# Kernel tuning notes

Hardware: AMD Instinct MI355X
Metric: run time of the kernel (lower is better)

## Reference

```python
import jax, jax.numpy as jnp
import numpy as np

NEG_INF = -jnp.inf


def setup_inputs() -> dict:
    B, T, E, H = 16, 1024, 1024, 1024  # batch, seq, embed_dim, head_dim (T <= H required by original buffer slicing)
    key = jax.random.key(0)
    k1, k2, k3, k4, k5, k6 = jax.random.split(key, 6)
    return {
        "key": jax.random.normal(k1, (B, T, E), dtype=jnp.float32),
        "query": jax.random.normal(k2, (B, T, E), dtype=jnp.float32),
        "value": jax.random.normal(k3, (B, T, E), dtype=jnp.float32),
        "padding_mask": jnp.zeros((B, 1, T), dtype=jnp.int32),
        # nn.Linear(embed_dim, head_dim, bias=False) weights: [head_dim, embed_dim]
        "Wk": jax.random.normal(k4, (H, E), dtype=jnp.float32) * (E ** -0.5),
        "Wq": jax.random.normal(k5, (H, E), dtype=jnp.float32) * (E ** -0.5),
        "Wv": jax.random.normal(k6, (H, E), dtype=jnp.float32) * (E ** -0.5),
    }


def reference(key, query, value, padding_mask, Wk, Wq, Wv):
    # key/query/value: [B, T, E]; W*: [H, E]
    B, T, E = key.shape
    k = jnp.einsum("bte,he->bth", key, Wk)
    q = jnp.einsum("bte,he->bth", query, Wq)
    v = jnp.einsum("bte,he->bth", value, Wv)
    # NOTE: original scales by d_k = key.size(-1) = embed_dim, not head_dim
    scale = 1.0 / jnp.sqrt(jnp.float32(E))
    qk = jnp.einsum("bth,bsh->bts", q, k) * scale  # [B, T, T]
    # causal buffer is tril(ones, diagonal=1): position i can attend to j <= i+1
    causal = jnp.tril(jnp.ones((T, T), dtype=jnp.float32), k=1)
    qk = jnp.where(causal == 0, NEG_INF, qk)
    qk = jnp.where(padding_mask == 1, NEG_INF, qk)  # padding_mask broadcasts [B,1,T] -> [B,T,T]
    p = jax.nn.softmax(qk, axis=-1)
    attn = jnp.einsum("bts,bsh->bth", p, v)  # dropout is identity in eval mode
    return attn
```

## Files before the change

### kernel.cpp

```cpp
#include <hip/hip_runtime.h>
#include <hip/hip_bf16.h>
#include <stdint.h>

typedef __bf16 bf16;
typedef __attribute__((ext_vector_type(8))) __bf16 bf16x8;
typedef __attribute__((ext_vector_type(4))) __bf16 bf16x4;
typedef __attribute__((ext_vector_type(4))) float  f32x4;

static __device__ __forceinline__ void gll16(const void* g, void* lds_base) {
  __builtin_amdgcn_global_load_lds((__attribute__((address_space(1))) void*)g,
                                   (__attribute__((address_space(3))) void*)lds_base,
                                   16, 0, 0);
}

#define BARR  __builtin_amdgcn_s_barrier()
#define VMW(N) asm volatile("s_waitcnt vmcnt(" #N ")" ::: "memory")
#define LGKM0 do { asm volatile("s_waitcnt lgkmcnt(0)" ::: "memory");          \
                   __builtin_amdgcn_sched_barrier(0); } while (0)

__global__ __launch_bounds__(512, 2) void proj8(const bf16* __restrict__ a0,
                                                const bf16* __restrict__ a1,
                                                const bf16* __restrict__ b0,
                                                const bf16* __restrict__ b1,
                                                bf16* __restrict__ c0,
                                                bf16* __restrict__ c1) {
  extern __shared__ char smem[];
  char* ldsA = smem;
  char* ldsB = smem + 65536;

  const int tid = threadIdx.x;
  const int lane = tid & 63, wave = tid >> 6;
  const int lo = lane & 15, hi = lane >> 4;
  const int wmi = wave >> 2, wni = wave & 3;
  const int swz = (lo & 7) << 4;

  const int nwg = gridDim.x;
  const int id = (blockIdx.x % 8) * (nwg >> 3) + blockIdx.x / 8;
  const int seg = id >> 8, idl = id & 255;
  const int row0 = (idl >> 2) * 256, col0 = (idl & 3) * 256;
  const bf16* Ap = (seg ? a1 : a0) + (size_t)row0 * 1024;
  const bf16* Bp = (seg ? b1 : b0) + (size_t)col0 * 1024;
  bf16* Cb = seg ? c1 : c0;

  const char* aSrc[2];
  const char* bSrc[2];
  int ldsOff[2];
#pragma unroll
  for (int rr = 0; rr < 2; ++rr) {
    const int x = rr * 8192 + tid * 16;
    const int lr = x >> 7;
    const int colx = (x & 127) ^ ((lr & 7) << 4);
    aSrc[rr] = (const char*)Ap + (size_t)(((lr >> 6) << 7) | (lr & 63)) * 2048 + colx;
    bSrc[rr] = (const char*)Bp + (size_t)(((lr >> 5) << 6) | (lr & 31)) * 2048 + colx;
    ldsOff[rr] = rr * 8192 + wave * 1024;
  }
  auto stA = [&](int h, int buf, int t) {
    const int tc = t > 15 ? 15 : t;
#pragma unroll
    for (int rr = 0; rr < 2; ++rr)
      gll16(aSrc[rr] + h * 131072 + tc * 128,
            ldsA + buf * 32768 + h * 16384 + ldsOff[rr]);
  };
  auto stB = [&](int h, int buf, int t) {
    const int tc = t > 15 ? 15 : t;
#pragma unroll
    for (int rr = 0; rr < 2; ++rr)
      gll16(bSrc[rr] + h * 65536 + tc * 128,
            ldsB + buf * 32768 + h * 16384 + ldsOff[rr]);
  };

  f32x4 acc[8][4] = {};
  bf16x8 af[4][2], bq0[2][2], bq1[2][2];

  auto rdA = [&](int mq, int buf) {
#pragma unroll
    for (int i = 0; i < 4; ++i) {
      const int lr = wmi * 64 + i * 16 + lo;
#pragma unroll
      for (int kh = 0; kh < 2; ++kh)
        af[i][kh] = *(const bf16x8*)(ldsA + buf * 32768 + mq * 16384 +
                                     lr * 128 + ((kh * 64 + hi * 16) ^ swz));
    }
  };
  auto rdB = [&](bf16x8 bq[2][2], int nq, int buf) {
#pragma unroll
    for (int n = 0; n < 2; ++n) {
      const int lr = wni * 32 + n * 16 + lo;
#pragma unroll
      for (int kh = 0; kh < 2; ++kh)
        bq[n][kh] = *(const bf16x8*)(ldsB + buf * 32768 + nq * 16384 +
                                     lr * 128 + ((kh * 64 + hi * 16) ^ swz));
    }
  };
  auto mma = [&](bf16x8 bq[2][2], int mq, int nq) {
    __builtin_amdgcn_s_setprio(1);
#pragma unroll
    for (int i = 0; i < 4; ++i)
#pragma unroll
      for (int n = 0; n < 2; ++n)
#pragma unroll
        for (int kh = 0; kh < 2; ++kh)
          acc[mq * 4 + i][nq * 2 + n] = __builtin_amdgcn_mfma_f32_16x16x32_bf16(
              af[i][kh], bq[n][kh], acc[mq * 4 + i][nq * 2 + n], 0, 0, 0);
    __builtin_amdgcn_s_setprio(0);
  };

  stA(0, 0, 0); stB(1, 0, 0); stA(1, 0, 0); stB(0, 0, 0);
  stA(0, 1, 1); stB(1, 1, 1); stA(1, 1, 1);
  VMW(6); BARR;

  for (int j = 0; j < 8; ++j) {
    const int t1 = 2 * j + 1, t2 = 2 * j + 2, t3 = 2 * j + 3;
    rdA(0, 0); rdB(bq0, 0, 0); stB(0, 1, t1);
    BARR; LGKM0; mma(bq0, 0, 0); BARR;
    rdB(bq1, 1, 0); stA(0, 0, t2);
    BARR; LGKM0; mma(bq1, 0, 1); BARR;
    rdA(1, 0); stB(1, 0, t2);
    BARR; LGKM0; mma(bq1, 1, 1); BARR;
    stA(1, 0, t2);
    BARR; LGKM0; mma(bq0, 1, 0); VMW(6); BARR;
    rdA(0, 1); rdB(bq0, 0, 1); stB(0, 0, t2);
    BARR; LGKM0; mma(bq0, 0, 0); BARR;
    rdB(bq1, 1, 1); stA(0, 1, t3);
    BARR; LGKM0; mma(bq1, 0, 1); BARR;
    rdA(1, 1); stB(1, 1, t3);
    BARR; LGKM0; mma(bq1, 1, 1); BARR;
    stA(1, 1, t3);
    BARR; LGKM0; mma(bq0, 1, 0); VMW(6); BARR;
  }

  if (!seg) {
#pragma unroll
    for (int m = 0; m < 8; ++m)
#pragma unroll
      for (int n = 0; n < 4; ++n) {
        const int c = col0 + wni * 64 + n * 16 + lo;
        const int rbase = row0 + wmi * 128 + m * 16 + hi * 4;
#pragma unroll
        for (int j = 0; j < 4; ++j)
          Cb[(size_t)(rbase + j) * 1024 + c] = (bf16)acc[m][n][j];
      }
  } else {
#pragma unroll
    for (int m = 0; m < 8; ++m)
#pragma unroll
      for (int n = 0; n < 4; ++n) {
        const int r = row0 + wmi * 128 + m * 16 + hi * 4;
        const int c = col0 + wni * 64 + n * 16 + lo;
        const int bb = r >> 10, tt = r & 1023;
        bf16x4 h = { (bf16)acc[m][n][0], (bf16)acc[m][n][1],
                     (bf16)acc[m][n][2], (bf16)acc[m][n][3] };
        *(bf16x4*)(Cb + ((size_t)bb << 20) + ((size_t)c << 10) + tt) = h;
      }
  }
  asm volatile("s_waitcnt vmcnt(0)" ::: "memory");
}

template <int VARIANT>
__global__ __launch_bounds__(512, 2) void gemm8(const bf16* __restrict__ a0,
                                                const bf16* __restrict__ b0,
                                                bf16* __restrict__ c0,
                                                float* __restrict__ Cf,
                                                const int* __restrict__ pad) {
  constexpr int TM = (VARIANT == 0) ? 256 : 128;
  constexpr int TN = (VARIANT == 0) ? 256 : 128;
  constexpr int ABYTES = TM * 64;
  constexpr int BBYTES = TN * 64;
  constexpr int AROUNDS = ABYTES / 8192;
  constexpr int BROUNDS = BBYTES / 8192;
  constexpr int FI = TM / 64;
  constexpr int FN = TN / 64;
  extern __shared__ char smem[];
  char* ldsA = smem;
  char* ldsB = smem + 2 * ABYTES;

  const int tid = threadIdx.x;
  const int lane = tid & 63, wave = tid >> 6;
  const int lo = lane & 15, hi = lane >> 4;
  const int wmi = wave >> 2, wni = wave & 3;
  const int swz = ((lo >> 1) & 3) << 4;

  const int nwg = gridDim.x;
  const int id = (blockIdx.x % 8) * (nwg >> 3) + blockIdx.x / 8;

  int row0, col0, nt, batch = 0;
  const bf16 *Ap, *Bp;
  bf16* Cb;
  if (VARIANT == 0) {
    const int idl = id & 255;
    row0 = (idl >> 2) * 256; col0 = (idl & 3) * 256; nt = 32;
    Ap = a0 + (size_t)row0 * 1024;
    Bp = b0 + (size_t)col0 * 1024;
    Cb = c0;
  } else {
    batch = id >> 6;
    const int it = (id >> 3) & 7, jt = id & 7;
    row0 = it * 128; col0 = jt * 128;
    nt = (VARIANT == 3) ? min(32, 4 * it + 5) : 32;
    if (VARIANT == 2 && jt >= it + 2) {
      bf16* Sb = c0 + ((size_t)batch << 20);
      bf16x8 z = {};
#pragma unroll
      for (int q = 0; q < (TM * TN) / (512 * 8); ++q) {
        const int off = (q * 512 + tid) * 8;
        *(bf16x8*)(Sb + (size_t)(row0 + (off >> 7)) * 1024 + col0 + (off & 127)) = z;
      }
      return;
    }
    Ap = a0 + ((size_t)batch << 20) + (size_t)row0 * 1024;
    Bp = b0 + ((size_t)batch << 20) + (size_t)col0 * 1024;
    Cb = c0;
  }
  const int ntm1 = nt - 1;

  auto stgA = [&](int tidx, int slot) {
    const int tc = tidx > ntm1 ? ntm1 : tidx;
#pragma unroll
    for (int r = 0; r < AROUNDS; ++r) {
      const int x  = (r * 512 + tid) * 16;
      const int xs = x ^ (((x >> 7) & 3) << 4);
      gll16((const char*)Ap + (size_t)(xs >> 6) * 2048 + (size_t)tc * 64 + (xs & 63),
            ldsA + slot * ABYTES + r * 8192 + wave * 1024);
    }
  };
  auto stgB = [&](int tidx, int slot) {
    const int tc = tidx > ntm1 ? ntm1 : tidx;
#pragma unroll
    for (int r = 0; r < BROUNDS; ++r) {
      const int x  = (r * 512 + tid) * 16;
      const int xs = x ^ (((x >> 7) & 3) << 4);
      gll16((const char*)Bp + (size_t)(xs >> 6) * 2048 + (size_t)tc * 64 + (xs & 63),
            ldsB + slot * BBYTES + r * 8192 + wave * 1024);
    }
  };

  f32x4 acc[2 * FI][FN] = {};
  bf16x8 af[FI], bfr[FN];

  auto rdA = [&](int mh, int slot) {
#pragma unroll
    for (int i = 0; i < FI; ++i) {
      const int row = wmi * (TM / 2) + mh * (TM / 4) + i * 16 + lo;
      af[i] = *(const bf16x8*)(ldsA + slot * ABYTES + ((row * 64 + hi * 16) ^ swz));
    }
  };
  auto rdB = [&](int slot) {
#pragma unroll
    for (int n = 0; n < FN; ++n) {
      const int row = wni * (TN / 4) + n * 16 + lo;
      bfr[n] = *(const bf16x8*)(ldsB + slot * BBYTES + ((row * 64 + hi * 16) ^ swz));
    }
  };
  auto mmaQ = [&](int mh) {
    __builtin_amdgcn_s_setprio(1);
#pragma unroll
    for (int i = 0; i < FI; ++i)
#pragma unroll
      for (int n = 0; n < FN; ++n)
        acc[mh * FI + i][n] = __builtin_amdgcn_mfma_f32_16x16x32_bf16(
            af[i], bfr[n], acc[mh * FI + i][n], 0, 0, 0);
    __builtin_amdgcn_s_setprio(0);
  };

  stgB(0, 0);
  stgA(0, 0);
  stgB(1, 1);
  if constexpr (BROUNDS == 2) { VMW(2); } else { VMW(1); }
  BARR;

#pragma unroll 2
  for (int u = 0; u < nt; ++u) {
    const int cur = u & 1;
    rdA(0, cur);
    rdB(cur);
    stgA(u + 1, cur ^ 1);
    BARR; LGKM0;
    mmaQ(0);
    BARR;
    rdA(1, cur);
    stgB(u + 2, cur);
    BARR; LGKM0;
    mmaQ(1);
    if constexpr (BROUNDS == 2) { VMW(2); } else { VMW(1); }
    BARR;
  }

  if (VARIANT == 0) {
#pragma unroll
    for (int m = 0; m < 2 * FI; ++m)
#pragma unroll
      for (int n = 0; n < FN; ++n) {
        const int c = col0 + wni * (TN / 4) + n * 16 + lo;
        const int rbase = row0 + wmi * (TM / 2) + m * 16 + hi * 4;
#pragma unroll
        for (int j = 0; j < 4; ++j)
          Cb[(size_t)(rbase + j) * 1024 + c] = (bf16)acc[m][n][j];
      }
  } else if (VARIANT == 2) {
    const float NINF = -__builtin_inff();
#pragma unroll
    for (int n = 0; n < FN; ++n) {
      const int s = col0 + wni * (TN / 4) + n * 16 + lo;
      const int pd = pad[(batch << 10) + s];
#pragma unroll
      for (int m = 0; m < 2 * FI; ++m) {
        const int tbase = row0 + wmi * (TM / 2) + m * 16 + hi * 4;
#pragma unroll
        for (int j = 0; j < 4; ++j) {
          float v = acc[m][n][j] * 0.03125f;
          if (s > tbase + j + 1) v = 0.f;
          else if (pd != 0) v = NINF;
          Cb[((size_t)batch << 20) + (size_t)(tbase + j) * 1024 + s] = (bf16)v;
        }
      }
    }
  } else {
#pragma unroll
    for (int m = 0; m < 2 * FI; ++m)
#pragma unroll
      for (int n = 0; n < FN; ++n) {
        const int h2 = col0 + wni * (TN / 4) + n * 16 + lo;
        const int tbase = row0 + wmi * (TM / 2) + m * 16 + hi * 4;
#pragma unroll
        for (int j = 0; j < 4; ++j)
          Cf[((size_t)batch << 20) + (size_t)(tbase + j) * 1024 + h2] = acc[m][n][j];
      }
  }
  asm volatile("s_waitcnt vmcnt(0)" ::: "memory");
}

__global__ __launch_bounds__(256) void cvt3_kernel(const float* __restrict__ s0,
                                                   const float* __restrict__ s1,
                                                   const float* __restrict__ s2,
                                                   bf16* __restrict__ d0,
                                                   bf16* __restrict__ d1,
                                                   bf16* __restrict__ d2) {
  const int seg = blockIdx.x >> 13, blk = blockIdx.x & 8191;
  const float* src = seg == 0 ? s0 : (seg == 1 ? s1 : s2);
  bf16* dst = seg == 0 ? d0 : (seg == 1 ? d1 : d2);
  const int i = (blk * 256 + threadIdx.x) * 8;
  const f32x4 a = *(const f32x4*)(src + i);
  const f32x4 b = *(const f32x4*)(src + i + 4);
  bf16x8 o = { (bf16)a[0], (bf16)a[1], (bf16)a[2], (bf16)a[3],
               (bf16)b[0], (bf16)b[1], (bf16)b[2], (bf16)b[3] };
  *(bf16x8*)(dst + i) = o;
}

__global__ __launch_bounds__(256) void cvtWT_kernel(const float* __restrict__ Wq,
                                                    const float* __restrict__ Wk,
                                                    const float* __restrict__ Wv,
                                                    bf16* __restrict__ WqT,
                                                    bf16* __restrict__ WkT,
                                                    bf16* __restrict__ Wvb) {
  const int t = threadIdx.x;
  if (blockIdx.x >= 512) {
    const int i = ((blockIdx.x - 512) * 256 + t) * 8;
    const f32x4 a = *(const f32x4*)(Wv + i);
    const f32x4 b = *(const f32x4*)(Wv + i + 4);
    bf16x8 o = { (bf16)a[0], (bf16)a[1], (bf16)a[2], (bf16)a[3],
                 (bf16)b[0], (bf16)b[1], (bf16)b[2], (bf16)b[3] };
    *(bf16x8*)(Wvb + i) = o;
    return;
  }
  const int m = blockIdx.x >> 8;
  const float* src = m ? Wk : Wq;
  bf16* dst = m ? WkT : WqT;
  const int tile = blockIdx.x & 255;
  const int tr = (tile >> 4) * 64, tc = (tile & 15) * 64;
  __shared__ bf16 s[64][72];
#pragma unroll
  for (int it = 0; it < 4; ++it) {
    const int row = it * 16 + (t >> 4), col = (t & 15) * 4;
    const f32x4 v = *(const f32x4*)(src + (size_t)(tr + row) * 1024 + tc + col);
#pragma unroll
    for (int j = 0; j < 4; ++j) s[col + j][row] = (bf16)v[j];
  }
  __syncthreads();
  const int c = t >> 2, rb = (t & 3) * 16;
  bf16* d = dst + (size_t)(tc + c) * 1024 + tr + rb;
  *(bf16x8*)(d)     = *(const bf16x8*)&s[c][rb];
  *(bf16x8*)(d + 8) = *(const bf16x8*)&s[c][rb + 8];
}

__global__ __launch_bounds__(256) void softmax_kernel(bf16* __restrict__ S) {
  const int row  = blockIdx.x * 4 + (threadIdx.x >> 6);
  const int lane = threadIdx.x & 63;
  const int t = row & 1023;
  const int w = min(1024, t + 2);
  const bool act = lane * 16 < w;
  bf16* r = S + (size_t)row * 1024 + lane * 16;
  bf16x8 v0 = {}, v1 = {};
  float f[16];
#pragma unroll
  for (int j = 0; j < 16; ++j) f[j] = -1e30f;
  if (act) {
    v0 = *(const bf16x8*)r;
    v1 = *(const bf16x8*)(r + 8);
#pragma unroll
    for (int j = 0; j < 16; ++j)
      if (lane * 16 + j < w) f[j] = (float)(j < 8 ? v0[j] : v1[j - 8]);
  }
  float m = f[0];
#pragma unroll
  for (int j = 1; j < 16; ++j) m = fmaxf(m, f[j]);
#pragma unroll
  for (int o = 32; o; o >>= 1) m = fmaxf(m, __shfl_xor(m, o, 64));
  float sum = 0.f;
  float e[16];
#pragma unroll
  for (int j = 0; j < 16; ++j) { e[j] = __expf(f[j] - m); sum += e[j]; }
#pragma unroll
  for (int o = 32; o; o >>= 1) sum += __shfl_xor(sum, o, 64);
  const float inv = 1.0f / sum;
  if (act) {
#pragma unroll
    for (int j = 0; j < 8; ++j) {
      v0[j] = (bf16)(lane * 16 + j < w ? e[j] * inv : 0.f);
      v1[j] = (bf16)(lane * 16 + 8 + j < w ? e[8 + j] * inv : 0.f);
    }
    *(bf16x8*)r = v0;
    *(bf16x8*)(r + 8) = v1;
  }
}

extern "C" void kernel_launch(void* const* d_in, const int* in_sizes, int n_in,
                              void* d_out, int out_size, void* d_ws, size_t ws_size,
                              hipStream_t stream) {
  const float* key   = (const float*)d_in[0];
  const float* query = (const float*)d_in[1];
  const float* value = (const float*)d_in[2];
  const int*   pad   = (const int*)d_in[3];
  const float* Wk    = (const float*)d_in[4];
  const float* Wq    = (const float*)d_in[5];
  const float* Wv    = (const float*)d_in[6];
  float* out = (float*)d_out;

  bf16* WqT = (bf16*)d_ws;
  bf16* WkT = WqT + (1 << 20);
  bf16* Wvb = WkT + (1 << 20);
  bf16* P   = Wvb + (1 << 20);
  bf16* Y   = P   + (1 << 20);
  bf16* vT  = Y   + (16 << 20);
  bf16* S   = vT  + (16 << 20);
  bf16* Xq  = S;
  bf16* Xk  = (bf16*)d_out;
  bf16* Xv  = Xk + (16 << 20);

  hipFuncSetAttribute(reinterpret_cast<const void*>(&proj8),
                      hipFuncAttributeMaxDynamicSharedMemorySize, 131072);
  hipFuncSetAttribute(reinterpret_cast<const void*>(&gemm8<0>),
                      hipFuncAttributeMaxDynamicSharedMemorySize, 65536);
  hipFuncSetAttribute(reinterpret_cast<const void*>(&gemm8<2>),
                      hipFuncAttributeMaxDynamicSharedMemorySize, 32768);
  hipFuncSetAttribute(reinterpret_cast<const void*>(&gemm8<3>),
                      hipFuncAttributeMaxDynamicSharedMemorySize, 32768);

  cvtWT_kernel<<<1024, 256, 0, stream>>>(Wq, Wk, Wv, WqT, WkT, Wvb);
  gemm8<0><<<16, 512, 65536, stream>>>(WkT, WqT, P, nullptr, nullptr);
  cvt3_kernel<<<24576, 256, 0, stream>>>(query, key, value, Xq, Xk, Xv);

  proj8<<<512, 512, 131072, stream>>>(Xq, Xv, P, Wvb, Y, vT);

  gemm8<2><<<1024, 512, 32768, stream>>>(Y, Xk, S, nullptr, pad);
  softmax_kernel<<<4096, 256, 0, stream>>>(S);
  gemm8<3><<<1024, 512, 32768, stream>>>(S, vT, nullptr, out, nullptr);
}
```

Measured before the change: 237.3 us.

## Fuse weight-product GEMM into the input conversion kernel launch

Merges the small 16-block WkT·WqT GEMM into the fp32→bf16 conversion kernel as extra blocks in one grid, and specializes gemm8 to 128x128 tiles only. This removes a separate launch and lets the GEMM run alongside the memory-bound conversion. Every block now reserves 64KB of dynamic LDS, which may limit how many conversion blocks are resident per CU. The GEMM blocks could also become a tail if they are scheduled late.

```diff
diff --git a/kernel.cpp b/kernel.cpp
--- a/kernel.cpp
+++ b/kernel.cpp
@@ -162,12 +162,9 @@
                                                 bf16* __restrict__ c0,
                                                 float* __restrict__ Cf,
                                                 const int* __restrict__ pad) {
-  constexpr int TM = (VARIANT == 0) ? 256 : 128;
-  constexpr int TN = (VARIANT == 0) ? 256 : 128;
+  constexpr int TM = 128, TN = 128;
   constexpr int ABYTES = TM * 64;
   constexpr int BBYTES = TN * 64;
-  constexpr int AROUNDS = ABYTES / 8192;
-  constexpr int BROUNDS = BBYTES / 8192;
   constexpr int FI = TM / 64;
   constexpr int FN = TN / 64;
   extern __shared__ char smem[];
@@ -183,55 +180,38 @@
   const int nwg = gridDim.x;
   const int id = (blockIdx.x % 8) * (nwg >> 3) + blockIdx.x / 8;
 
-  int row0, col0, nt, batch = 0;
-  const bf16 *Ap, *Bp;
-  bf16* Cb;
-  if (VARIANT == 0) {
-    const int idl = id & 255;
-    row0 = (idl >> 2) * 256; col0 = (idl & 3) * 256; nt = 32;
-    Ap = a0 + (size_t)row0 * 1024;
-    Bp = b0 + (size_t)col0 * 1024;
-    Cb = c0;
-  } else {
-    batch = id >> 6;
-    const int it = (id >> 3) & 7, jt = id & 7;
-    row0 = it * 128; col0 = jt * 128;
-    nt = (VARIANT == 3) ? min(32, 4 * it + 5) : 32;
-    if (VARIANT == 2 && jt >= it + 2) {
-      bf16* Sb = c0 + ((size_t)batch << 20);
-      bf16x8 z = {};
-#pragma unroll
-      for (int q = 0; q < (TM * TN) / (512 * 8); ++q) {
-        const int off = (q * 512 + tid) * 8;
-        *(bf16x8*)(Sb + (size_t)(row0 + (off >> 7)) * 1024 + col0 + (off & 127)) = z;
-      }
-      return;
-    }
-    Ap = a0 + ((size_t)batch << 20) + (size_t)row0 * 1024;
-    Bp = b0 + ((size_t)batch << 20) + (size_t)col0 * 1024;
-    Cb = c0;
-  }
+  const int batch = id >> 6;
+  const int it = (id >> 3) & 7, jt = id & 7;
+  const int row0 = it * 128, col0 = jt * 128;
+  const int nt = (VARIANT == 3) ? min(32, 4 * it + 5) : 32;
+  if (VARIANT == 2 && jt >= it + 2) {
+    bf16* Sb = c0 + ((size_t)batch << 20);
+    bf16x8 z = {};
+#pragma unroll
+    for (int q = 0; q < (TM * TN) / (512 * 8); ++q) {
+      const int off = (q * 512 + tid) * 8;
+      *(bf16x8*)(Sb + (size_t)(row0 + (off >> 7)) * 1024 + col0 + (off & 127)) = z;
+    }
+    return;
+  }
+  const bf16* Ap = a0 + ((size_t)batch << 20) + (size_t)row0 * 1024;
+  const bf16* Bp = b0 + ((size_t)batch << 20) + (size_t)col0 * 1024;
+  bf16* Cb = c0;
   const int ntm1 = nt - 1;
 
   auto stgA = [&](int tidx, int slot) {
     const int tc = tidx > ntm1 ? ntm1 : tidx;
-#pragma unroll
-    for (int r = 0; r < AROUNDS; ++r) {
-      const int x  = (r * 512 + tid) * 16;
-      const int xs = x ^ (((x >> 7) & 3) << 4);
-      gll16((const char*)Ap + (size_t)(xs >> 6) * 2048 + (size_t)tc * 64 + (xs & 63),
-            ldsA + slot * ABYTES + r * 8192 + wave * 1024);
-    }
+    const int x  = tid * 16;
+    const int xs = x ^ (((x >> 7) & 3) << 4);
+    gll16((const char*)Ap + (size_t)(xs >> 6) * 2048 + (size_t)tc * 64 + (xs & 63),
+          ldsA + slot * ABYTES + wave * 1024);
   };
   auto stgB = [&](int tidx, int slot) {
     const int tc = tidx > ntm1 ? ntm1 : tidx;
-#pragma unroll
-    for (int r = 0; r < BROUNDS; ++r) {
-      const int x  = (r * 512 + tid) * 16;
-      const int xs = x ^ (((x >> 7) & 3) << 4);
-      gll16((const char*)Bp + (size_t)(xs >> 6) * 2048 + (size_t)tc * 64 + (xs & 63),
-            ldsB + slot * BBYTES + r * 8192 + wave * 1024);
-    }
+    const int x  = tid * 16;
+    const int xs = x ^ (((x >> 7) & 3) << 4);
+    gll16((const char*)Bp + (size_t)(xs >> 6) * 2048 + (size_t)tc * 64 + (xs & 63),
+          ldsB + slot * BBYTES + wave * 1024);
   };
 
   f32x4 acc[2 * FI][FN] = {};
@@ -265,7 +245,7 @@
   stgB(0, 0);
   stgA(0, 0);
   stgB(1, 1);
-  if constexpr (BROUNDS == 2) { VMW(2); } else { VMW(1); }
+  VMW(1);
   BARR;
 
 #pragma unroll 2
@@ -281,22 +261,11 @@
     stgB(u + 2, cur);
     BARR; LGKM0;
     mmaQ(1);
-    if constexpr (BROUNDS == 2) { VMW(2); } else { VMW(1); }
+    VMW(1);
     BARR;
   }
 
-  if (VARIANT == 0) {
-#pragma unroll
-    for (int m = 0; m < 2 * FI; ++m)
-#pragma unroll
-      for (int n = 0; n < FN; ++n) {
-        const int c = col0 + wni * (TN / 4) + n * 16 + lo;
-        const int rbase = row0 + wmi * (TM / 2) + m * 16 + hi * 4;
-#pragma unroll
-        for (int j = 0; j < 4; ++j)
-          Cb[(size_t)(rbase + j) * 1024 + c] = (bf16)acc[m][n][j];
-      }
-  } else if (VARIANT == 2) {
+  if (VARIANT == 2) {
     const float NINF = -__builtin_inff();
 #pragma unroll
     for (int n = 0; n < FN; ++n) {
@@ -329,21 +298,119 @@
   asm volatile("s_waitcnt vmcnt(0)" ::: "memory");
 }
 
-__global__ __launch_bounds__(256) void cvt3_kernel(const float* __restrict__ s0,
-                                                   const float* __restrict__ s1,
-                                                   const float* __restrict__ s2,
-                                                   bf16* __restrict__ d0,
-                                                   bf16* __restrict__ d1,
-                                                   bf16* __restrict__ d2) {
-  const int seg = blockIdx.x >> 13, blk = blockIdx.x & 8191;
-  const float* src = seg == 0 ? s0 : (seg == 1 ? s1 : s2);
-  bf16* dst = seg == 0 ? d0 : (seg == 1 ? d1 : d2);
-  const int i = (blk * 256 + threadIdx.x) * 8;
-  const f32x4 a = *(const f32x4*)(src + i);
-  const f32x4 b = *(const f32x4*)(src + i + 4);
-  bf16x8 o = { (bf16)a[0], (bf16)a[1], (bf16)a[2], (bf16)a[3],
-               (bf16)b[0], (bf16)b[1], (bf16)b[2], (bf16)b[3] };
-  *(bf16x8*)(dst + i) = o;
+__global__ __launch_bounds__(512, 2) void cvtP_kernel(const float* __restrict__ s0,
+                                                      const float* __restrict__ s1,
+                                                      const float* __restrict__ s2,
+                                                      bf16* __restrict__ d0,
+                                                      bf16* __restrict__ d1,
+                                                      bf16* __restrict__ d2,
+                                                      const bf16* __restrict__ WkT,
+                                                      const bf16* __restrict__ WqT,
+                                                      bf16* __restrict__ P) {
+  extern __shared__ char smem[];
+  const int nwg = gridDim.x;
+  const int id = (blockIdx.x % 8) * (nwg >> 3) + blockIdx.x / 8;
+  const int tid = threadIdx.x;
+
+  if (id < 12288) {
+    const int seg = id / 4096, blk = id % 4096;
+    const float* src = seg == 0 ? s0 : (seg == 1 ? s1 : s2);
+    bf16* dst = seg == 0 ? d0 : (seg == 1 ? d1 : d2);
+    const int i = (blk * 512 + tid) * 8;
+    const f32x4 a = *(const f32x4*)(src + i);
+    const f32x4 b = *(const f32x4*)(src + i + 4);
+    bf16x8 o = { (bf16)a[0], (bf16)a[1], (bf16)a[2], (bf16)a[3],
+                 (bf16)b[0], (bf16)b[1], (bf16)b[2], (bf16)b[3] };
+    *(bf16x8*)(dst + i) = o;
+    return;
+  }
+
+  constexpr int ABYTES = 16384;
+  char* ldsA = smem;
+  char* ldsB = smem + 2 * ABYTES;
+  const int lane = tid & 63, wave = tid >> 6;
+  const int lo = lane & 15, hi = lane >> 4;
+  const int wmi = wave >> 2, wni = wave & 3;
+  const int swz = ((lo >> 1) & 3) << 4;
+
+  const int idl = id - 12288;
+  const int row0 = (idl >> 2) * 256, col0 = (idl & 3) * 256;
+  const bf16* Ap = WkT + (size_t)row0 * 1024;
+  const bf16* Bp = WqT + (size_t)col0 * 1024;
+
+  auto stg = [&](const bf16* base, char* ldsOp, int tidx, int slot) {
+    const int tc = tidx > 31 ? 31 : tidx;
+#pragma unroll
+    for (int r = 0; r < 2; ++r) {
+      const int x  = (r * 512 + tid) * 16;
+      const int xs = x ^ (((x >> 7) & 3) << 4);
+      gll16((const char*)base + (size_t)(xs >> 6) * 2048 + (size_t)tc * 64 + (xs & 63),
+            ldsOp + slot * ABYTES + r * 8192 + wave * 1024);
+    }
+  };
+
+  f32x4 acc[8][4] = {};
+  bf16x8 af[4], bfr[4];
+
+  auto rdA = [&](int mh, int slot) {
+#pragma unroll
+    for (int i = 0; i < 4; ++i) {
+      const int row = wmi * 128 + mh * 64 + i * 16 + lo;
+      af[i] = *(const bf16x8*)(ldsA + slot * ABYTES + ((row * 64 + hi * 16) ^ swz));
+    }
+  };
+  auto rdB = [&](int slot) {
+#pragma unroll
+    for (int n = 0; n < 4; ++n) {
+      const int row = wni * 64 + n * 16 + lo;
+      bfr[n] = *(const bf16x8*)(ldsB + slot * ABYTES + ((row * 64 + hi * 16) ^ swz));
+    }
+  };
+  auto mmaQ = [&](int mh) {
+    __builtin_amdgcn_s_setprio(1);
+#pragma unroll
+    for (int i = 0; i < 4; ++i)
+#pragma unroll
+      for (int n = 0; n < 4; ++n)
+        acc[mh * 4 + i][n] = __builtin_amdgcn_mfma_f32_16x16x32_bf16(
+            af[i], bfr[n], acc[mh * 4 + i][n], 0, 0, 0);
+    __builtin_amdgcn_s_setprio(0);
+  };
+
+  stg(Bp, ldsB, 0, 0);
+  stg(Ap, ldsA, 0, 0);
+  stg(Bp, ldsB, 1, 1);
+  VMW(2);
+  BARR;
+
+#pragma unroll 2
+  for (int u = 0; u < 32; ++u) {
+    const int cur = u & 1;
+    rdA(0, cur);
+    rdB(cur);
+    stg(Ap, ldsA, u + 1, cur ^ 1);
+    BARR; LGKM0;
+    mmaQ(0);
+    BARR;
+    rdA(1, cur);
+    stg(Bp, ldsB, u + 2, cur);
+    BARR; LGKM0;
+    mmaQ(1);
+    VMW(2);
+    BARR;
+  }
+
+#pragma unroll
+  for (int m = 0; m < 8; ++m)
+#pragma unroll
+    for (int n = 0; n < 4; ++n) {
+      const int c = col0 + wni * 64 + n * 16 + lo;
+      const int rbase = row0 + wmi * 128 + m * 16 + hi * 4;
+#pragma unroll
+      for (int j = 0; j < 4; ++j)
+        P[(size_t)(rbase + j) * 1024 + c] = (bf16)acc[m][n][j];
+    }
+  asm volatile("s_waitcnt vmcnt(0)" ::: "memory");
 }
 
 __global__ __launch_bounds__(256) void cvtWT_kernel(const float* __restrict__ Wq,
@@ -448,7 +515,7 @@
 
   hipFuncSetAttribute(reinterpret_cast<const void*>(&proj8),
                       hipFuncAttributeMaxDynamicSharedMemorySize, 131072);
-  hipFuncSetAttribute(reinterpret_cast<const void*>(&gemm8<0>),
+  hipFuncSetAttribute(reinterpret_cast<const void*>(&cvtP_kernel),
                       hipFuncAttributeMaxDynamicSharedMemorySize, 65536);
   hipFuncSetAttribute(reinterpret_cast<const void*>(&gemm8<2>),
                       hipFuncAttributeMaxDynamicSharedMemorySize, 32768);
@@ -456,8 +523,8 @@
                       hipFuncAttributeMaxDynamicSharedMemorySize, 32768);
 
   cvtWT_kernel<<<1024, 256, 0, stream>>>(Wq, Wk, Wv, WqT, WkT, Wvb);
-  gemm8<0><<<16, 512, 65536, stream>>>(WkT, WqT, P, nullptr, nullptr);
-  cvt3_kernel<<<24576, 256, 0, stream>>>(query, key, value, Xq, Xk, Xv);
+  cvtP_kernel<<<12304, 512, 65536, stream>>>(query, key, value, Xq, Xk, Xv,
+                                             WkT, WqT, P);
 
   proj8<<<512, 512, 131072, stream>>>(Xq, Xv, P, Wvb, Y, vT);
 
```

Measured after the change: 248.9 us. 4.9% more time.
